# Kernel tuning notes

Measured on AMD Instinct MI355X. Metric: run time of the kernel, lower is better.

The kernel has to match this reference:

```python
import jax, jax.numpy as jnp
import numpy as np

NB_CLASSES = 10  # matches init_kwargs nb_classes


def setup_inputs() -> dict:
    key = jax.random.key(0)
    k1, k2 = jax.random.split(key)
    N, D = 500_000, 64
    h = jax.random.normal(k1, (N, D), dtype=jnp.float32)
    yhat = jax.random.randint(k2, (N,), 0, NB_CLASSES, dtype=jnp.int32)
    return {"h": h, "yhat": yhat}


def reference(h, yhat):
    # Original torch loop: for each class k, gather h_k = h[yhat==k],
    # M_k = mean_i(h_i h_i^T) * 0.5 + I, loss += 0.5 * logdet(M_k).
    # mean of outer products == (masked h)^T @ h / count_k, so we avoid
    # the ragged gather and any [N, D, D] intermediate entirely.
    N, D = h.shape
    eye = jnp.eye(D, dtype=h.dtype)

    def class_term(k):
        mask = (yhat == k).astype(h.dtype)            # [N]
        count = jnp.sum(mask)                         # B_k
        gram = jnp.einsum('nd,ne->de', mask[:, None] * h, h)  # sum_i h_i h_i^T
        M = gram * (0.5 / count) + eye                # [D, D], SPD
        _, logabsdet = jnp.linalg.slogdet(M)
        return 0.5 * logabsdet

    # NB_CLASSES is a small fixed constant -> Python loop is fine & keeps
    # peak memory at one extra [N, D] buffer.
    return jnp.sum(jnp.stack([class_term(k) for k in range(NB_CLASSES)]))
```

## Files before the change

### kernel.cpp

```cpp
#include <hip/hip_runtime.h>
#include <hip/hip_bf16.h>

typedef __attribute__((ext_vector_type(8))) short    short8;
typedef __attribute__((ext_vector_type(4))) float    f32x4;
typedef __attribute__((ext_vector_type(4))) _Float16 f16x4;
typedef __attribute__((ext_vector_type(2))) unsigned u32x2;

#define NCLS 10
#define TILE 64
#define TPB  512
#define NQ   10
#define PPB  (NCLS * NQ * 256)
#define CH   16

#define AS1 __attribute__((address_space(1)))
#define AS3 __attribute__((address_space(3)))

#define MF(a, b, c) __builtin_amdgcn_mfma_f32_16x16x32_bf16((a), (b), (c), 0, 0, 0)

static __device__ __forceinline__ unsigned pkh2(float a, float b) {
    unsigned short ha = __builtin_bit_cast(unsigned short, (_Float16)a);
    unsigned short hb = __builtin_bit_cast(unsigned short, (_Float16)b);
    return (unsigned)ha | ((unsigned)hb << 16);
}

static __device__ __forceinline__ void compute_tile(
        const char* hsb, const char* mkb, int cls, int xcls, int wq,
        int hi, int col, f32x4 (&acc)[NQ], f32x4 (&accx)[3]) {
    const int s56 = (col & 3) << 4;
    const int s6  = (col & 4) << 4;
    const char* rb0 = hsb + col * 128 + ((hi * 16) ^ s56) + s6;
    const char* rb1 = hsb + col * 128 + ((hi * 16) ^ s56) + (64 ^ s6);
    const char* mb  = mkb + cls  * 128 + hi * 16;
    const char* xb  = mkb + xcls * 128 + hi * 16;

#pragma unroll
    for (int ks = 0; ks < 2; ++ks) {
        const char* rb = ks ? rb1 : rb0;
        const short8 m = *(const short8*)(mb + ks * 64);
        short8 raw[4], am[4];
#pragma unroll
        for (int nb = 0; nb < 4; ++nb) {
            raw[nb] = *(const short8*)(rb + nb * 2048);
            am[nb]  = raw[nb] & m;
        }
        acc[0] = MF(am[0], am[0], acc[0]);
        acc[1] = MF(am[0], am[1], acc[1]);
        acc[2] = MF(am[0], am[2], acc[2]);
        acc[3] = MF(am[0], am[3], acc[3]);
        acc[4] = MF(am[1], am[1], acc[4]);
        acc[5] = MF(am[1], am[2], acc[5]);
        acc[6] = MF(am[1], am[3], acc[6]);
        acc[7] = MF(am[2], am[2], acc[7]);
        acc[8] = MF(am[2], am[3], acc[8]);
        acc[9] = MF(am[3], am[3], acc[9]);

        const short8 mx = *(const short8*)(xb + ks * 64);
        switch (wq) {
        case 0: { short8 x0 = raw[0] & mx, x1 = raw[1] & mx;
                  accx[0] = MF(x0, x0, accx[0]);
                  accx[1] = MF(x0, x1, accx[1]);
                  accx[2] = MF(x1, x1, accx[2]); } break;
        case 1: { short8 x0 = raw[0] & mx, x2 = raw[2] & mx, x3 = raw[3] & mx;
                  accx[0] = MF(x0, x2, accx[0]);
                  accx[1] = MF(x0, x3, accx[1]); } break;
        case 2: { short8 x1 = raw[1] & mx, x2 = raw[2] & mx, x3 = raw[3] & mx;
                  accx[0] = MF(x1, x2, accx[0]);
                  accx[1] = MF(x1, x3, accx[1]);
                  accx[2] = MF(x2, x2, accx[2]); } break;
        default:{ short8 x2 = raw[2] & mx, x3 = raw[3] & mx;
                  accx[0] = MF(x2, x3, accx[0]);
                  accx[1] = MF(x3, x3, accx[1]); } break;
        }
    }
}

__global__ __launch_bounds__(TPB, 4) void HL_gram(
        const float* __restrict__ h, const int* __restrict__ yhat,
        _Float16* __restrict__ partials, int* __restrict__ cntp,
        int N, int ntiles, int G) {
    __shared__ __align__(16) float          fs[2][TILE * 64];
    __shared__ __align__(16) unsigned short hs[2][64 * TILE];
    __shared__ __align__(16) unsigned short mk[2][NCLS * TILE];
    __shared__ __align__(16) int            ylds[2][TILE];

    const int tid  = threadIdx.x;
    const int wid  = tid >> 6;
    const int lane = tid & 63;
    const int hi   = lane >> 4;
    const int col  = lane & 15;

    const int cls  = wid;
    const int xcls = 8 + (wid >> 2);
    const int wq   = wid & 3;

    f32x4 acc[NQ], accx[3];
#pragma unroll
    for (int q = 0; q < NQ; ++q) acc[q] = (f32x4){0.f, 0.f, 0.f, 0.f};
#pragma unroll
    for (int q = 0; q < 3; ++q)  accx[q] = (f32x4){0.f, 0.f, 0.f, 0.f};
    int c0=0,c1=0,c2=0,c3=0,c4=0,c5=0,c6=0,c7=0,c8=0,c9=0;

    const int bid = blockIdx.x;
    const int K   = (ntiles - bid + G - 1) / G;

    const unsigned step   = (unsigned)G * TILE * 256u;
    const unsigned maxoff = (unsigned)(N - 1) * 256u + (unsigned)(tid & 15) * 16u;
    unsigned off0 = ((unsigned)bid * TILE + (unsigned)(tid >> 4)) * 256u
                    + (unsigned)(tid & 15) * 16u;
    const unsigned ystep  = (unsigned)G * TILE * 4u;
    const unsigned maxy   = (unsigned)(N - 4) * 4u;
    unsigned offy = (unsigned)bid * 256u + (unsigned)lane * 16u;
    int rowN = bid * TILE + lane;

    char* fdst0 = (char*)&fs[0][0] + wid * 1024;
    char* fdst1 = (char*)&fs[1][0] + wid * 1024;

    {
        unsigned o0 = off0 > maxoff ? maxoff : off0;
        unsigned o1 = off0 + 8192u; o1 = o1 > maxoff ? maxoff : o1;
        __builtin_amdgcn_global_load_lds((const AS1 float*)((const char*)h + o0),
                                         (AS3 float*)fdst0, 16, 0, 0);
        __builtin_amdgcn_global_load_lds((const AS1 float*)((const char*)h + o1),
                                         (AS3 float*)(fdst0 + 8192), 16, 0, 0);
        if (wid == 7 && lane < 16) {
            unsigned oy = offy > maxy ? maxy : offy;
            __builtin_amdgcn_global_load_lds((const AS1 int*)((const char*)yhat + oy),
                                             (AS3 int*)&ylds[0][0], 16, 0, 0);
        }
        off0 += step; offy += ystep;
    }

    for (int k = 0; k < K; ++k) {
        const int slot = k & 1;

        asm volatile("s_waitcnt vmcnt(0)" ::: "memory");
        asm volatile("s_waitcnt lgkmcnt(0)" ::: "memory");
        __builtin_amdgcn_s_barrier();
        __builtin_amdgcn_sched_barrier(0);

        if (k + 1 < K) {
            char* fd = slot ? fdst0 : fdst1;
            unsigned o0 = off0 > maxoff ? maxoff : off0;
            unsigned o1 = off0 + 8192u; o1 = o1 > maxoff ? maxoff : o1;
            __builtin_amdgcn_global_load_lds((const AS1 float*)((const char*)h + o0),
                                             (AS3 float*)fd, 16, 0, 0);
            __builtin_amdgcn_global_load_lds((const AS1 float*)((const char*)h + o1),
                                             (AS3 float*)(fd + 8192), 16, 0, 0);
            if (wid == 7 && lane < 16) {
                unsigned oy = offy > maxy ? maxy : offy;
                __builtin_amdgcn_global_load_lds((const AS1 int*)((const char*)yhat + oy),
                                                 (AS3 int*)&ylds[slot ^ 1][0], 16, 0, 0);
            }
            off0 += step; offy += ystep;
        }

        const float* fsb = &fs[slot][0];
        const char*  hsw = (const char*)&hs[slot][0];
        const char*  hsr = (const char*)&hs[slot ^ 1][0];
        const char*  mkw = (const char*)&mk[slot][0];
        const char*  mkr = (const char*)&mk[slot ^ 1][0];

        if (wid & 1) {
            {
                const float* fp = fsb + (wid * 8) * 64 + lane;
                float x[8];
#pragma unroll
                for (int j = 0; j < 8; ++j) x[j] = fp[j * 64];
                u32x2 lo, hi2;
                lo[0]  = pkh2(0,0);
                unsigned w0, w1, w2, w3;
                {
                    __hip_bfloat162 p0 = __float22bfloat162_rn(make_float2(x[0], x[1]));
                    __hip_bfloat162 p1 = __float22bfloat162_rn(make_float2(x[2], x[3]));
                    __hip_bfloat162 p2 = __float22bfloat162_rn(make_float2(x[4], x[5]));
                    __hip_bfloat162 p3 = __float22bfloat162_rn(make_float2(x[6], x[7]));
                    __builtin_memcpy(&w0, &p0, 4); __builtin_memcpy(&w1, &p1, 4);
                    __builtin_memcpy(&w2, &p2, 4); __builtin_memcpy(&w3, &p3, 4);
                }
                lo[0] = w0; lo[1] = w1; hi2[0] = w2; hi2[1] = w3;
                char* hb = (char*)hsw + lane * 128 + ((wid * 16) ^ ((lane & 7) << 4));
                *(u32x2*)hb       = lo;
                *(u32x2*)(hb + 8) = hi2;
            }
            if (wid == 7) {
                int y = ylds[slot][lane];
                if (rowN >= N) y = -1;
                unsigned short* mbw = (unsigned short*)mkw;
#pragma unroll
                for (int c = 0; c < NCLS; ++c)
                    mbw[c * TILE + lane] = (y == c) ? (unsigned short)0xFFFFu
                                                    : (unsigned short)0u;
                c0 += (int)__popcll(__ballot(y == 0));
                c1 += (int)__popcll(__ballot(y == 1));
                c2 += (int)__popcll(__ballot(y == 2));
                c3 += (int)__popcll(__ballot(y == 3));
                c4 += (int)__popcll(__ballot(y == 4));
                c5 += (int)__popcll(__ballot(y == 5));
                c6 += (int)__popcll(__ballot(y == 6));
                c7 += (int)__popcll(__ballot(y == 7));
                c8 += (int)__popcll(__ballot(y == 8));
                c9 += (int)__popcll(__ballot(y == 9));
                rowN += G * TILE;
            }
            if (k > 0)
                compute_tile(hsr, mkr, cls, xcls, wq, hi, col, acc, accx);
        } else {
            if (k > 0)
                compute_tile(hsr, mkr, cls, xcls, wq, hi, col, acc, accx);
            {
                const float* fp = fsb + (wid * 8) * 64 + lane;
                float x[8];
#pragma unroll
                for (int j = 0; j < 8; ++j) x[j] = fp[j * 64];
                unsigned w0, w1, w2, w3;
                {
                    __hip_bfloat162 p0 = __float22bfloat162_rn(make_float2(x[0], x[1]));
                    __hip_bfloat162 p1 = __float22bfloat162_rn(make_float2(x[2], x[3]));
                    __hip_bfloat162 p2 = __float22bfloat162_rn(make_float2(x[4], x[5]));
                    __hip_bfloat162 p3 = __float22bfloat162_rn(make_float2(x[6], x[7]));
                    __builtin_memcpy(&w0, &p0, 4); __builtin_memcpy(&w1, &p1, 4);
                    __builtin_memcpy(&w2, &p2, 4); __builtin_memcpy(&w3, &p3, 4);
                }
                u32x2 lo, hi2;
                lo[0] = w0; lo[1] = w1; hi2[0] = w2; hi2[1] = w3;
                char* hb = (char*)hsw + lane * 128 + ((wid * 16) ^ ((lane & 7) << 4));
                *(u32x2*)hb       = lo;
                *(u32x2*)(hb + 8) = hi2;
            }
        }
    }

    asm volatile("s_waitcnt lgkmcnt(0)" ::: "memory");
    __builtin_amdgcn_s_barrier();
    __builtin_amdgcn_sched_barrier(0);
    compute_tile((const char*)&hs[(K - 1) & 1][0], (const char*)&mk[(K - 1) & 1][0],
                 cls, xcls, wq, hi, col, acc, accx);

    _Float16* pb = partials + (size_t)bid * PPB;
    {
        _Float16* po = pb + (size_t)cls * (NQ * 256);
#pragma unroll
        for (int q = 0; q < NQ; ++q) {
            u32x2 pk; pk[0] = pkh2(acc[q][0], acc[q][1]);
            pk[1] = pkh2(acc[q][2], acc[q][3]);
            *(u32x2*)(po + q * 256 + (lane << 2)) = pk;
        }
    }
    {
        _Float16* px = pb + (size_t)xcls * (NQ * 256) + (lane << 2);
        u32x2 pk0, pk1, pk2;
        pk0[0] = pkh2(accx[0][0], accx[0][1]); pk0[1] = pkh2(accx[0][2], accx[0][3]);
        pk1[0] = pkh2(accx[1][0], accx[1][1]); pk1[1] = pkh2(accx[1][2], accx[1][3]);
        pk2[0] = pkh2(accx[2][0], accx[2][1]); pk2[1] = pkh2(accx[2][2], accx[2][3]);
        switch (wq) {
        case 0: *(u32x2*)(px + 0 * 256) = pk0;
                *(u32x2*)(px + 1 * 256) = pk1;
                *(u32x2*)(px + 4 * 256) = pk2; break;
        case 1: *(u32x2*)(px + 2 * 256) = pk0;
                *(u32x2*)(px + 3 * 256) = pk1; break;
        case 2: *(u32x2*)(px + 5 * 256) = pk0;
                *(u32x2*)(px + 6 * 256) = pk1;
                *(u32x2*)(px + 7 * 256) = pk2; break;
        default:*(u32x2*)(px + 8 * 256) = pk0;
                *(u32x2*)(px + 9 * 256) = pk1; break;
        }
    }
    if (wid == 7 && lane == 0) {
        int* cp = cntp + bid * 16;
        cp[0]=c0; cp[1]=c1; cp[2]=c2; cp[3]=c3; cp[4]=c4;
        cp[5]=c5; cp[6]=c6; cp[7]=c7; cp[8]=c8; cp[9]=c9;
    }
}

__global__ void HL_reduce(const _Float16* __restrict__ partials, float* __restrict__ rpart,
                          float* __restrict__ out, int G, int CS) {
    const int idx = blockIdx.x * blockDim.x + threadIdx.x;
    if (blockIdx.x == 0 && threadIdx.x == 0) out[0] = 0.f;
    if (idx >= CH * NCLS * NQ * 64) return;
    const int ch = idx / (NCLS * NQ * 64);
    const int r  = idx % (NCLS * NQ * 64);
    const int cq = r >> 6;
    const int l  = r & 63;

    int b0 = ch * CS;
    int b1 = b0 + CS; if (b1 > G) b1 = G;

    f32x4 s = (f32x4){0.f, 0.f, 0.f, 0.f};
    const _Float16* p = partials + (size_t)cq * 256 + (l << 2);
    for (int b = b0; b < b1; ++b) {
        f16x4 v = *(const f16x4*)(p + (size_t)b * PPB);
        s[0] += (float)v[0]; s[1] += (float)v[1];
        s[2] += (float)v[2]; s[3] += (float)v[3];
    }
    *reinterpret_cast<f32x4*>(rpart + ((size_t)ch * (NCLS * NQ) + cq) * 256 + (l << 2)) = s;
}

__global__ __launch_bounds__(64, 1) void HL_chol(
        const float* __restrict__ rpart, const int* __restrict__ cntp,
        float* __restrict__ out, int G) {
    __shared__ float M[64][68];
    __shared__ float lcol[64];
    const int cls = blockIdx.x;
    const int i   = threadIdx.x;

    int c = 0;
    for (int b = i; b < G; b += 64) c += cntp[b * 16 + cls];
#pragma unroll
    for (int off = 32; off > 0; off >>= 1) c += __shfl_xor(c, off);
    const float inv = 0.5f / (float)c;

    const int QMB[NQ] = {0,0,0,0,1,1,1,2,2,3};
    const int QNB[NQ] = {0,1,2,3,1,2,3,2,3,3};
    const float* rp = rpart + (size_t)cls * (NQ * 256);
#pragma unroll
    for (int q = 0; q < NQ; ++q) {
        f32x4 s = (f32x4){0.f, 0.f, 0.f, 0.f};
#pragma unroll
        for (int ch = 0; ch < CH; ++ch)
            s += *reinterpret_cast<const f32x4*>(rp + (size_t)ch * (NCLS * NQ * 256) + q * 256 + (i << 2));
        const int row0 = QMB[q] * 16 + ((i >> 4) << 2);
        const int colo = QNB[q] * 16 + (i & 15);
#pragma unroll
        for (int rr = 0; rr < 4; ++rr) {
            M[row0 + rr][colo] = s[rr];
            M[colo][row0 + rr] = s[rr];
        }
    }
    __syncthreads();

    float row[64];
#pragma unroll
    for (int c2 = 0; c2 < 64; ++c2)
        row[c2] = M[i][c2] * inv + (c2 == i ? 1.0f : 0.0f);

#pragma unroll
    for (int j = 0; j < 64; ++j) {
        const float piv = __shfl(row[j], j);
        const float li  = row[j] * rsqrtf(piv);
        lcol[i] = li;
        __syncthreads();
#pragma unroll
        for (int c2 = j + 1; c2 < 64; ++c2)
            row[c2] -= li * lcol[c2];
        __syncthreads();
    }

    float slog = 0.f;
#pragma unroll
    for (int j = 0; j < 64; ++j)
        if (i == j) slog = __logf(row[j]);
    slog += __shfl_down(slog, 32); slog += __shfl_down(slog, 16);
    slog += __shfl_down(slog, 8);  slog += __shfl_down(slog, 4);
    slog += __shfl_down(slog, 2);  slog += __shfl_down(slog, 1);
    if (i == 0) atomicAdd(out, 0.5f * slog);
}

extern "C" void kernel_launch(void* const* d_in, const int* in_sizes, int n_in,
                              void* d_out, int out_size, void* d_ws, size_t ws_size,
                              hipStream_t stream) {
    const float* h    = (const float*)d_in[0];
    const int*   yhat = (const int*)d_in[1];
    const int    N    = in_sizes[1];
    float* out = (float*)d_out;

    const size_t rpart_sz = (size_t)CH * NCLS * NQ * 256 * sizeof(float);
    const size_t cntp_off = rpart_sz;

    const int ntiles = (N + TILE - 1) / TILE;
    int G = 512;
    {
        const size_t perG = 64 + (size_t)PPB * sizeof(_Float16);
        if (ws_size > rpart_sz) {
            size_t maxG = (ws_size - rpart_sz) / perG;
            if ((size_t)G > maxG) G = (int)maxG;
        } else G = 1;
        if (G < 1) G = 1;
    }
    if (G > ntiles) G = ntiles;

    const size_t partials_off = cntp_off + (size_t)G * 16 * sizeof(int);
    float*    rpart    = (float*)d_ws;
    int*      cntp     = (int*)((char*)d_ws + cntp_off);
    _Float16* partials = (_Float16*)((char*)d_ws + partials_off);

    HL_gram<<<G, TPB, 0, stream>>>(h, yhat, partials, cntp, N, ntiles, G);

    int CS = (G + CH - 1) / CH;
    const int rthreads = CH * NCLS * NQ * 64;
    HL_reduce<<<(rthreads + 255) / 256, 256, 0, stream>>>(partials, rpart, out, G, CS);

    HL_chol<<<NCLS, 64, 0, stream>>>(rpart, cntp, out, G);
}
```

Measured before the change: 90.38 us.

## Compute class masks in-register from yhat instead of staging LDS mask tiles

Removes the shared-memory mask tiles written by wave 7 and the associated per-class ballot counting. Each wave now reads the raw labels from a 4-deep label buffer, builds its cls/xcls masks and counts in registers, and reduces counts with shuffles. It also unifies the odd/even wave paths so every wave converts then computes, and wraps MFMA sections in s_setprio. This trades LDS mask traffic and the wave-7 imbalance for extra per-lane compare ALU work, and drops the convert/compute interleaving between even and odd waves.

```diff
diff --git a/kernel.cpp b/kernel.cpp
--- a/kernel.cpp
+++ b/kernel.cpp
@@ -5,6 +5,7 @@
 typedef __attribute__((ext_vector_type(4))) float    f32x4;
 typedef __attribute__((ext_vector_type(4))) _Float16 f16x4;
 typedef __attribute__((ext_vector_type(2))) unsigned u32x2;
+typedef __attribute__((ext_vector_type(4))) int      i32x4;
 
 #define NCLS 10
 #define TILE 64
@@ -18,32 +19,74 @@
 
 #define MF(a, b, c) __builtin_amdgcn_mfma_f32_16x16x32_bf16((a), (b), (c), 0, 0, 0)
 
+static __device__ __forceinline__ unsigned pkbf2(float a, float b) {
+    __hip_bfloat162 p = __float22bfloat162_rn(make_float2(a, b));
+    unsigned u; __builtin_memcpy(&u, &p, 4);
+    return u;
+}
 static __device__ __forceinline__ unsigned pkh2(float a, float b) {
     unsigned short ha = __builtin_bit_cast(unsigned short, (_Float16)a);
     unsigned short hb = __builtin_bit_cast(unsigned short, (_Float16)b);
     return (unsigned)ha | ((unsigned)hb << 16);
 }
+static __device__ __forceinline__ unsigned umin2(unsigned a, unsigned b) {
+    return a < b ? a : b;
+}
 
 static __device__ __forceinline__ void compute_tile(
-        const char* hsb, const char* mkb, int cls, int xcls, int wq,
-        int hi, int col, f32x4 (&acc)[NQ], f32x4 (&accx)[3]) {
+        const char* hsb, const char* yb, int vr,
+        int cls, int xcls, int wq, int hi, int col,
+        f32x4 (&acc)[NQ], f32x4 (&accx)[3], int& cnt, int& cntx) {
     const int s56 = (col & 3) << 4;
     const int s6  = (col & 4) << 4;
     const char* rb0 = hsb + col * 128 + ((hi * 16) ^ s56) + s6;
     const char* rb1 = hsb + col * 128 + ((hi * 16) ^ s56) + (64 ^ s6);
-    const char* mb  = mkb + cls  * 128 + hi * 16;
-    const char* xb  = mkb + xcls * 128 + hi * 16;
 
 #pragma unroll
     for (int ks = 0; ks < 2; ++ks) {
-        const char* rb = ks ? rb1 : rb0;
-        const short8 m = *(const short8*)(mb + ks * 64);
+        const char* rb   = ks ? rb1 : rb0;
+        const int   krow = ks * 32 + hi * 8;
+
+        i32x4 ya = *(const i32x4*)(yb + ks * 128 + hi * 32);
+        i32x4 yc = *(const i32x4*)(yb + ks * 128 + hi * 32 + 16);
+        ya[0] = (krow + 0 < vr) ? ya[0] : -1;
+        ya[1] = (krow + 1 < vr) ? ya[1] : -1;
+        ya[2] = (krow + 2 < vr) ? ya[2] : -1;
+        ya[3] = (krow + 3 < vr) ? ya[3] : -1;
+        yc[0] = (krow + 4 < vr) ? yc[0] : -1;
+        yc[1] = (krow + 5 < vr) ? yc[1] : -1;
+        yc[2] = (krow + 6 < vr) ? yc[2] : -1;
+        yc[3] = (krow + 7 < vr) ? yc[3] : -1;
+
+        short8 m, mx;
+        m[0] = (ya[0] == cls) ? (short)-1 : (short)0;
+        m[1] = (ya[1] == cls) ? (short)-1 : (short)0;
+        m[2] = (ya[2] == cls) ? (short)-1 : (short)0;
+        m[3] = (ya[3] == cls) ? (short)-1 : (short)0;
+        m[4] = (yc[0] == cls) ? (short)-1 : (short)0;
+        m[5] = (yc[1] == cls) ? (short)-1 : (short)0;
+        m[6] = (yc[2] == cls) ? (short)-1 : (short)0;
+        m[7] = (yc[3] == cls) ? (short)-1 : (short)0;
+        mx[0] = (ya[0] == xcls) ? (short)-1 : (short)0;
+        mx[1] = (ya[1] == xcls) ? (short)-1 : (short)0;
+        mx[2] = (ya[2] == xcls) ? (short)-1 : (short)0;
+        mx[3] = (ya[3] == xcls) ? (short)-1 : (short)0;
+        mx[4] = (yc[0] == xcls) ? (short)-1 : (short)0;
+        mx[5] = (yc[1] == xcls) ? (short)-1 : (short)0;
+        mx[6] = (yc[2] == xcls) ? (short)-1 : (short)0;
+        mx[7] = (yc[3] == xcls) ? (short)-1 : (short)0;
+        cnt  += (ya[0] == cls)  + (ya[1] == cls)  + (ya[2] == cls)  + (ya[3] == cls)
+              + (yc[0] == cls)  + (yc[1] == cls)  + (yc[2] == cls)  + (yc[3] == cls);
+        cntx += (ya[0] == xcls) + (ya[1] == xcls) + (ya[2] == xcls) + (ya[3] == xcls)
+              + (yc[0] == xcls) + (yc[1] == xcls) + (yc[2] == xcls) + (yc[3] == xcls);
+
         short8 raw[4], am[4];
 #pragma unroll
         for (int nb = 0; nb < 4; ++nb) {
             raw[nb] = *(const short8*)(rb + nb * 2048);
             am[nb]  = raw[nb] & m;
         }
+        __builtin_amdgcn_s_setprio(1);
         acc[0] = MF(am[0], am[0], acc[0]);
         acc[1] = MF(am[0], am[1], acc[1]);
         acc[2] = MF(am[0], am[2], acc[2]);
@@ -54,8 +97,6 @@
         acc[7] = MF(am[2], am[2], acc[7]);
         acc[8] = MF(am[2], am[3], acc[8]);
         acc[9] = MF(am[3], am[3], acc[9]);
-
-        const short8 mx = *(const short8*)(xb + ks * 64);
         switch (wq) {
         case 0: { short8 x0 = raw[0] & mx, x1 = raw[1] & mx;
                   accx[0] = MF(x0, x0, accx[0]);
@@ -72,6 +113,7 @@
                   accx[0] = MF(x2, x3, accx[0]);
                   accx[1] = MF(x3, x3, accx[1]); } break;
         }
+        __builtin_amdgcn_s_setprio(0);
     }
 }
 
@@ -81,8 +123,7 @@
         int N, int ntiles, int G) {
     __shared__ __align__(16) float          fs[2][TILE * 64];
     __shared__ __align__(16) unsigned short hs[2][64 * TILE];
-    __shared__ __align__(16) unsigned short mk[2][NCLS * TILE];
-    __shared__ __align__(16) int            ylds[2][TILE];
+    __shared__ __align__(16) int            ylds[4][TILE];
 
     const int tid  = threadIdx.x;
     const int wid  = tid >> 6;
@@ -99,36 +140,35 @@
     for (int q = 0; q < NQ; ++q) acc[q] = (f32x4){0.f, 0.f, 0.f, 0.f};
 #pragma unroll
     for (int q = 0; q < 3; ++q)  accx[q] = (f32x4){0.f, 0.f, 0.f, 0.f};
-    int c0=0,c1=0,c2=0,c3=0,c4=0,c5=0,c6=0,c7=0,c8=0,c9=0;
+    int cnt = 0, cntx = 0;
 
     const int bid = blockIdx.x;
     const int K   = (ntiles - bid + G - 1) / G;
 
-    const unsigned step   = (unsigned)G * TILE * 256u;
-    const unsigned maxoff = (unsigned)(N - 1) * 256u + (unsigned)(tid & 15) * 16u;
-    unsigned off0 = ((unsigned)bid * TILE + (unsigned)(tid >> 4)) * 256u
-                    + (unsigned)(tid & 15) * 16u;
-    const unsigned ystep  = (unsigned)G * TILE * 4u;
-    const unsigned maxy   = (unsigned)(N - 4) * 4u;
-    unsigned offy = (unsigned)bid * 256u + (unsigned)lane * 16u;
-    int rowN = bid * TILE + lane;
+    const unsigned step  = (unsigned)G * (TILE * 256u);
+    const unsigned maxh  = (unsigned)(N - 1) * 256u + (unsigned)(tid & 15) * 16u;
+    unsigned offh = ((unsigned)bid * TILE + (unsigned)(tid >> 4)) * 256u
+                  + (unsigned)(tid & 15) * 16u;
+    const unsigned ystep = (unsigned)G * (TILE * 4u);
+    const unsigned maxy  = (unsigned)(N - 4) * 4u;
+    unsigned offy = (unsigned)bid * (TILE * 4u) + (unsigned)lane * 16u;
 
     char* fdst0 = (char*)&fs[0][0] + wid * 1024;
     char* fdst1 = (char*)&fs[1][0] + wid * 1024;
 
     {
-        unsigned o0 = off0 > maxoff ? maxoff : off0;
-        unsigned o1 = off0 + 8192u; o1 = o1 > maxoff ? maxoff : o1;
+        const unsigned o0 = umin2(offh, maxh);
+        const unsigned o1 = umin2(offh + 8192u, maxh);
         __builtin_amdgcn_global_load_lds((const AS1 float*)((const char*)h + o0),
                                          (AS3 float*)fdst0, 16, 0, 0);
         __builtin_amdgcn_global_load_lds((const AS1 float*)((const char*)h + o1),
                                          (AS3 float*)(fdst0 + 8192), 16, 0, 0);
         if (wid == 7 && lane < 16) {
-            unsigned oy = offy > maxy ? maxy : offy;
+            const unsigned oy = umin2(offy, maxy);
             __builtin_amdgcn_global_load_lds((const AS1 int*)((const char*)yhat + oy),
                                              (AS3 int*)&ylds[0][0], 16, 0, 0);
         }
-        off0 += step; offy += ystep;
+        offh += step; offy += ystep;
     }
 
     for (int k = 0; k < K; ++k) {
@@ -141,108 +181,58 @@
 
         if (k + 1 < K) {
             char* fd = slot ? fdst0 : fdst1;
-            unsigned o0 = off0 > maxoff ? maxoff : off0;
-            unsigned o1 = off0 + 8192u; o1 = o1 > maxoff ? maxoff : o1;
+            const unsigned o0 = umin2(offh, maxh);
+            const unsigned o1 = umin2(offh + 8192u, maxh);
             __builtin_amdgcn_global_load_lds((const AS1 float*)((const char*)h + o0),
                                              (AS3 float*)fd, 16, 0, 0);
             __builtin_amdgcn_global_load_lds((const AS1 float*)((const char*)h + o1),
                                              (AS3 float*)(fd + 8192), 16, 0, 0);
             if (wid == 7 && lane < 16) {
-                unsigned oy = offy > maxy ? maxy : offy;
+                const unsigned oy = umin2(offy, maxy);
                 __builtin_amdgcn_global_load_lds((const AS1 int*)((const char*)yhat + oy),
-                                                 (AS3 int*)&ylds[slot ^ 1][0], 16, 0, 0);
+                                                 (AS3 int*)&ylds[(k + 1) & 3][0], 16, 0, 0);
             }
-            off0 += step; offy += ystep;
-        }
-
-        const float* fsb = &fs[slot][0];
-        const char*  hsw = (const char*)&hs[slot][0];
-        const char*  hsr = (const char*)&hs[slot ^ 1][0];
-        const char*  mkw = (const char*)&mk[slot][0];
-        const char*  mkr = (const char*)&mk[slot ^ 1][0];
-
-        if (wid & 1) {
-            {
-                const float* fp = fsb + (wid * 8) * 64 + lane;
-                float x[8];
-#pragma unroll
-                for (int j = 0; j < 8; ++j) x[j] = fp[j * 64];
-                u32x2 lo, hi2;
-                lo[0]  = pkh2(0,0);
-                unsigned w0, w1, w2, w3;
-                {
-                    __hip_bfloat162 p0 = __float22bfloat162_rn(make_float2(x[0], x[1]));
-                    __hip_bfloat162 p1 = __float22bfloat162_rn(make_float2(x[2], x[3]));
-                    __hip_bfloat162 p2 = __float22bfloat162_rn(make_float2(x[4], x[5]));
-                    __hip_bfloat162 p3 = __float22bfloat162_rn(make_float2(x[6], x[7]));
-                    __builtin_memcpy(&w0, &p0, 4); __builtin_memcpy(&w1, &p1, 4);
-                    __builtin_memcpy(&w2, &p2, 4); __builtin_memcpy(&w3, &p3, 4);
-                }
-                lo[0] = w0; lo[1] = w1; hi2[0] = w2; hi2[1] = w3;
-                char* hb = (char*)hsw + lane * 128 + ((wid * 16) ^ ((lane & 7) << 4));
-                *(u32x2*)hb       = lo;
-                *(u32x2*)(hb + 8) = hi2;
-            }
-            if (wid == 7) {
-                int y = ylds[slot][lane];
-                if (rowN >= N) y = -1;
-                unsigned short* mbw = (unsigned short*)mkw;
-#pragma unroll
-                for (int c = 0; c < NCLS; ++c)
-                    mbw[c * TILE + lane] = (y == c) ? (unsigned short)0xFFFFu
-                                                    : (unsigned short)0u;
-                c0 += (int)__popcll(__ballot(y == 0));
-                c1 += (int)__popcll(__ballot(y == 1));
-                c2 += (int)__popcll(__ballot(y == 2));
-                c3 += (int)__popcll(__ballot(y == 3));
-                c4 += (int)__popcll(__ballot(y == 4));
-                c5 += (int)__popcll(__ballot(y == 5));
-                c6 += (int)__popcll(__ballot(y == 6));
-                c7 += (int)__popcll(__ballot(y == 7));
-                c8 += (int)__popcll(__ballot(y == 8));
-                c9 += (int)__popcll(__ballot(y == 9));
-                rowN += G * TILE;
-            }
-            if (k > 0)
-                compute_tile(hsr, mkr, cls, xcls, wq, hi, col, acc, accx);
-        } else {
-            if (k > 0)
-                compute_tile(hsr, mkr, cls, xcls, wq, hi, col, acc, accx);
-            {
-                const float* fp = fsb + (wid * 8) * 64 + lane;
-                float x[8];
-#pragma unroll
-                for (int j = 0; j < 8; ++j) x[j] = fp[j * 64];
-                unsigned w0, w1, w2, w3;
-                {
-                    __hip_bfloat162 p0 = __float22bfloat162_rn(make_float2(x[0], x[1]));
-                    __hip_bfloat162 p1 = __float22bfloat162_rn(make_float2(x[2], x[3]));
-                    __hip_bfloat162 p2 = __float22bfloat162_rn(make_float2(x[4], x[5]));
-                    __hip_bfloat162 p3 = __float22bfloat162_rn(make_float2(x[6], x[7]));
-                    __builtin_memcpy(&w0, &p0, 4); __builtin_memcpy(&w1, &p1, 4);
-                    __builtin_memcpy(&w2, &p2, 4); __builtin_memcpy(&w3, &p3, 4);
-                }
-                u32x2 lo, hi2;
-                lo[0] = w0; lo[1] = w1; hi2[0] = w2; hi2[1] = w3;
-                char* hb = (char*)hsw + lane * 128 + ((wid * 16) ^ ((lane & 7) << 4));
-                *(u32x2*)hb       = lo;
-                *(u32x2*)(hb + 8) = hi2;
-            }
+            offh += step; offy += ystep;
+        }
+
+        {
+            const float* fp = &fs[slot][0] + wid * 512 + lane;
+            const float x0 = fp[0],   x1 = fp[64],  x2 = fp[128], x3 = fp[192];
+            const float x4 = fp[256], x5 = fp[320], x6 = fp[384], x7 = fp[448];
+            u32x2 lo, hi2;
+            lo[0]  = pkbf2(x0, x1); lo[1]  = pkbf2(x2, x3);
+            hi2[0] = pkbf2(x4, x5); hi2[1] = pkbf2(x6, x7);
+            char* hb = (char*)&hs[slot][0] + lane * 128 + ((wid * 16) ^ ((lane & 7) << 4));
+            *(u32x2*)hb       = lo;
+            *(u32x2*)(hb + 8) = hi2;
+        }
+
+        if (k > 0) {
+            const int vr = N - (bid + (k - 1) * G) * TILE;
+            compute_tile((const char*)&hs[slot ^ 1][0], (const char*)&ylds[(k - 1) & 3][0],
+                         vr, cls, xcls, wq, hi, col, acc, accx, cnt, cntx);
         }
     }
 
     asm volatile("s_waitcnt lgkmcnt(0)" ::: "memory");
     __builtin_amdgcn_s_barrier();
     __builtin_amdgcn_sched_barrier(0);
-    compute_tile((const char*)&hs[(K - 1) & 1][0], (const char*)&mk[(K - 1) & 1][0],
-                 cls, xcls, wq, hi, col, acc, accx);
+    {
+        const int vr = N - (bid + (K - 1) * G) * TILE;
+        compute_tile((const char*)&hs[(K - 1) & 1][0], (const char*)&ylds[(K - 1) & 3][0],
+                     vr, cls, xcls, wq, hi, col, acc, accx, cnt, cntx);
+    }
+
+    cnt  += __shfl_xor(cnt, 16);  cnt  += __shfl_xor(cnt, 32);
+    cntx += __shfl_xor(cntx, 16); cntx += __shfl_xor(cntx, 32);
 
     _Float16* pb = partials + (size_t)bid * PPB;
     {
         _Float16* po = pb + (size_t)cls * (NQ * 256);
 #pragma unroll
         for (int q = 0; q < NQ; ++q) {
-            u32x2 pk; pk[0] = pkh2(acc[q][0], acc[q][1]);
+            u32x2 pk;
+            pk[0] = pkh2(acc[q][0], acc[q][1]);
             pk[1] = pkh2(acc[q][2], acc[q][3]);
             *(u32x2*)(po + q * 256 + (lane << 2)) = pk;
         }
@@ -266,10 +256,9 @@
                 *(u32x2*)(px + 9 * 256) = pk1; break;
         }
     }
-    if (wid == 7 && lane == 0) {
-        int* cp = cntp + bid * 16;
-        cp[0]=c0; cp[1]=c1; cp[2]=c2; cp[3]=c3; cp[4]=c4;
-        cp[5]=c5; cp[6]=c6; cp[7]=c7; cp[8]=c8; cp[9]=c9;
+    if (lane == 0) {
+        cntp[bid * 16 + cls] = cnt;
+        if (wq == 0) cntp[bid * 16 + xcls] = cntx;
     }
 }
 
```

New measurement: 140.1 us. +55.0%, slower.
